# Optimization experiments

Hardware: AMD Instinct MI355X
Metric: run time of the kernel (lower is better)

Reference implementation:

```python
import jax, jax.numpy as jnp
import numpy as np

N_EMBED = 384
NUM_HEADS = 6
HEAD_SIZE = N_EMBED // NUM_HEADS  # 64
B, T = 8, 2048


def setup_inputs() -> dict:
    key = jax.random.key(0)
    ks = jax.random.split(key, 8)
    s = 1.0 / np.sqrt(N_EMBED)
    query = jax.random.normal(ks[0], (B, T, N_EMBED), dtype=jnp.float32)
    key_t = jax.random.normal(ks[1], (B, T, N_EMBED), dtype=jnp.float32)
    value = jax.random.normal(ks[2], (B, T, N_EMBED), dtype=jnp.float32)
    # causal-style mask, broadcastable over (B, H)
    mask = jnp.tril(jnp.ones((T, T), dtype=jnp.int32))[None, None]
    Wk = jax.random.normal(ks[3], (N_EMBED, N_EMBED), dtype=jnp.float32) * s
    Wq = jax.random.normal(ks[4], (N_EMBED, N_EMBED), dtype=jnp.float32) * s
    Wv = jax.random.normal(ks[5], (N_EMBED, N_EMBED), dtype=jnp.float32) * s
    Wproj = jax.random.normal(ks[6], (N_EMBED, N_EMBED), dtype=jnp.float32) * s
    bproj = jnp.zeros((N_EMBED,), dtype=jnp.float32)
    return {"query": query, "key": key_t, "value": value, "mask": mask,
            "Wk": Wk, "Wq": Wq, "Wv": Wv, "Wproj": Wproj, "bproj": bproj}


def _split_heads(x):
    b, t, c = x.shape
    return x.reshape(b, t, NUM_HEADS, c // NUM_HEADS).transpose(0, 2, 1, 3)  # [B,H,T,D]


def reference(query, key, value, mask, Wk, Wq, Wv, Wproj, bproj):
    b, t, c = query.shape
    # NOTE: source swaps names: k = key_proj(query), q = query_proj(key)
    k = _split_heads(query @ Wk.T)
    q = _split_heads(key @ Wq.T)
    v = _split_heads(value @ Wv.T)
    # scale by full C (not head_size), as in the source
    wei = jnp.einsum("bhqd,bhkd->bhqk", q, k) * (c ** -0.5)
    # masked_fill with 0 BEFORE softmax (faithful to source)
    wei = jnp.where(mask == 0, jnp.float32(0.0), wei)
    wei = jax.nn.softmax(wei, axis=-1)
    out = jnp.einsum("bhqk,bhkd->bhqd", wei, v)
    out = out.transpose(0, 2, 1, 3).reshape(b, t, c)
    out = out @ Wproj.T + bproj  # dropout is identity at inference
    return out
```

## Files before the change

### kernel.cpp

```cpp
#include <hip/hip_runtime.h>
#include <hip/hip_bf16.h>
#include <type_traits>


#define TT 2048
#define CC 384
#define HH 6
#define DD 64
#define SCALE2 0.07362223f

#if __has_builtin(__builtin_amdgcn_exp2f)
#define EXP2(x) __builtin_amdgcn_exp2f(x)
#else
#define EXP2(x) exp2f(x)
#endif

typedef __bf16 bf16x8 __attribute__((ext_vector_type(8)));
typedef __bf16 bf16x4 __attribute__((ext_vector_type(4)));
typedef float f32x4 __attribute__((ext_vector_type(4)));

__device__ __forceinline__ int swz(int row, int byteInRow) {
    return row * 128 + (byteInRow ^ ((row & 7) << 4));
}

__global__ __launch_bounds__(256) void qkv_proj_kernel(
    const float* __restrict__ query, const float* __restrict__ key,
    const float* __restrict__ value, const float* __restrict__ Wk,
    const float* __restrict__ Wq, const float* __restrict__ Wv,
    __bf16* __restrict__ Kb, __bf16* __restrict__ Qb, __bf16* __restrict__ VTb)
{
    __shared__ __align__(16) char smem[49152];

    const int tid = threadIdx.x;
    const int wid = tid >> 6, lane = tid & 63;
    const int lrow = lane & 15, g = lane >> 4;
    const int pid = blockIdx.z;
    const int m0 = blockIdx.x * 128, n0 = blockIdx.y * 64;
    const float* X = (pid == 0) ? query : ((pid == 1) ? key : value);
    const float* W = (pid == 0) ? Wk : ((pid == 1) ? Wq : Wv);

    const int xrow = tid >> 4, xcol = (tid & 15) * 4;
    const float* xp = X + (size_t)(m0 + xrow) * CC + xcol;
    const float* wp = W + (size_t)(n0 + (tid >> 4)) * CC + xcol;

    f32x4 xr[8], wr[4];

    f32x4 acc[2][4];
#pragma unroll
    for (int i = 0; i < 2; ++i)
#pragma unroll
        for (int j = 0; j < 4; ++j) acc[i][j] = (f32x4){0.f, 0.f, 0.f, 0.f};

#pragma unroll
    for (int i = 0; i < 8; ++i) xr[i] = *(const f32x4*)(xp + (size_t)i * 16 * CC);
#pragma unroll
    for (int i = 0; i < 4; ++i) wr[i] = *(const f32x4*)(wp + (size_t)i * 16 * CC);
    {
        char* Xd = smem;
        char* Wd = smem + 32768;
#pragma unroll
        for (int i = 0; i < 8; ++i) {
            bf16x4 hh;
            hh[0] = (__bf16)xr[i][0]; hh[1] = (__bf16)xr[i][1];
            hh[2] = (__bf16)xr[i][2]; hh[3] = (__bf16)xr[i][3];
            *(bf16x4*)(Xd + swz(xrow + i * 16, xcol * 2)) = hh;
        }
#pragma unroll
        for (int i = 0; i < 4; ++i) {
            bf16x4 hh;
            hh[0] = (__bf16)wr[i][0]; hh[1] = (__bf16)wr[i][1];
            hh[2] = (__bf16)wr[i][2]; hh[3] = (__bf16)wr[i][3];
            *(bf16x4*)(Wd + swz((tid >> 4) + i * 16, xcol * 2)) = hh;
        }
    }
    __syncthreads();

    int cur = 0;
    for (int kk = 0; kk < 6; ++kk) {
        if (kk < 5) {
            const int k0 = (kk + 1) * 64;
#pragma unroll
            for (int i = 0; i < 8; ++i) xr[i] = *(const f32x4*)(xp + (size_t)i * 16 * CC + k0);
#pragma unroll
            for (int i = 0; i < 4; ++i) wr[i] = *(const f32x4*)(wp + (size_t)i * 16 * CC + k0);
        }
        const char* Xs = smem + cur * 16384;
        const char* Ws = smem + 32768 + cur * 8192;

        __builtin_amdgcn_s_setprio(1);
        if (pid < 2) {
#pragma unroll
            for (int kc = 0; kc < 2; ++kc) {
                int kb = kc * 64 + g * 16;
                bf16x8 a0 = *(bf16x8*)(Xs + swz(wid * 32 + lrow, kb));
                bf16x8 a1 = *(bf16x8*)(Xs + swz(wid * 32 + 16 + lrow, kb));
#pragma unroll
                for (int nf = 0; nf < 4; ++nf) {
                    bf16x8 b = *(bf16x8*)(Ws + swz(nf * 16 + lrow, kb));
                    acc[0][nf] = __builtin_amdgcn_mfma_f32_16x16x32_bf16(a0, b, acc[0][nf], 0, 0, 0);
                    acc[1][nf] = __builtin_amdgcn_mfma_f32_16x16x32_bf16(a1, b, acc[1][nf], 0, 0, 0);
                }
            }
        } else {
#pragma unroll
            for (int kc = 0; kc < 2; ++kc) {
                int kb = kc * 64 + g * 16;
                bf16x8 b0 = *(bf16x8*)(Xs + swz(wid * 32 + lrow, kb));
                bf16x8 b1 = *(bf16x8*)(Xs + swz(wid * 32 + 16 + lrow, kb));
#pragma unroll
                for (int nf = 0; nf < 4; ++nf) {
                    bf16x8 a = *(bf16x8*)(Ws + swz(nf * 16 + lrow, kb));
                    acc[0][nf] = __builtin_amdgcn_mfma_f32_16x16x32_bf16(a, b0, acc[0][nf], 0, 0, 0);
                    acc[1][nf] = __builtin_amdgcn_mfma_f32_16x16x32_bf16(a, b1, acc[1][nf], 0, 0, 0);
                }
            }
        }
        __builtin_amdgcn_s_setprio(0);

        if (kk < 5) {
            char* Xd = smem + (cur ^ 1) * 16384;
            char* Wd = smem + 32768 + (cur ^ 1) * 8192;
#pragma unroll
            for (int i = 0; i < 8; ++i) {
                bf16x4 hh;
                hh[0] = (__bf16)xr[i][0]; hh[1] = (__bf16)xr[i][1];
                hh[2] = (__bf16)xr[i][2]; hh[3] = (__bf16)xr[i][3];
                *(bf16x4*)(Xd + swz(xrow + i * 16, xcol * 2)) = hh;
            }
#pragma unroll
            for (int i = 0; i < 4; ++i) {
                bf16x4 hh;
                hh[0] = (__bf16)wr[i][0]; hh[1] = (__bf16)wr[i][1];
                hh[2] = (__bf16)wr[i][2]; hh[3] = (__bf16)wr[i][3];
                *(bf16x4*)(Wd + swz((tid >> 4) + i * 16, xcol * 2)) = hh;
            }
        }
        __syncthreads();
        cur ^= 1;
    }

    if (pid < 2) {
        __bf16* out = (pid == 0) ? Kb : Qb;
        const float sc = (pid == 1) ? SCALE2 : 1.0f;
#pragma unroll
        for (int mf = 0; mf < 2; ++mf)
#pragma unroll
            for (int nf = 0; nf < 4; ++nf)
#pragma unroll
                for (int r = 0; r < 4; ++r) {
                    int m = m0 + wid * 32 + mf * 16 + g * 4 + r;
                    int n = n0 + nf * 16 + lrow;
                    int b = m >> 11, t = m & 2047, h = n >> 6, d = n & 63;
                    out[((size_t)(b * HH + h) * TT + t) * DD + d] = (__bf16)(acc[mf][nf][r] * sc);
                }
    } else {
#pragma unroll
        for (int mf = 0; mf < 2; ++mf)
#pragma unroll
            for (int nf = 0; nf < 4; ++nf)
#pragma unroll
                for (int r = 0; r < 4; ++r) {
                    int n = n0 + nf * 16 + g * 4 + r;
                    int m = m0 + wid * 32 + mf * 16 + lrow;
                    int b = m >> 11, t = m & 2047, h = n >> 6, d = n & 63;
                    VTb[((size_t)(b * HH + h) * DD + d) * TT + t] = (__bf16)acc[mf][nf][r];
                }
    }
}

__global__ __launch_bounds__(256) void suffix_kernel(
    const __bf16* __restrict__ VTb, float* __restrict__ Ssuf)
{
    __shared__ float tsum[4][32];
    const int bh = blockIdx.x;
    const int tid = threadIdx.x, wid = tid >> 6, lane = tid & 63;

#pragma unroll
    for (int it = 0; it < 4; ++it) {
        const int dr = blockIdx.y * 16 + wid * 4 + it;
        const __bf16* src = VTb + (size_t)(bh * DD + dr) * TT;
#pragma unroll
        for (int step = 0; step < 4; ++step) {
            bf16x8 v = *(const bf16x8*)(src + step * 512 + lane * 8);
            float sacc = 0.f;
#pragma unroll
            for (int i = 0; i < 8; ++i) sacc += (float)v[i];
            sacc += __shfl_xor(sacc, 1);
            sacc += __shfl_xor(sacc, 2);
            sacc += __shfl_xor(sacc, 4);
            if ((lane & 7) == 0) tsum[wid][step * 8 + (lane >> 3)] = sacc;
        }
        float s2 = 0.f;
        for (int j = 0; j < 32; ++j) {
            float tv = tsum[wid][j];
            if (j >= lane) s2 += tv;
        }
        if (lane <= 32) Ssuf[(size_t)(bh * 33 + lane) * 64 + dr] = s2;
    }
}

__global__ __launch_bounds__(256, 3) void attn_kernel(
    const __bf16* __restrict__ Qb, const __bf16* __restrict__ Kb,
    const __bf16* __restrict__ VTb, const float* __restrict__ Ssuf,
    __bf16* __restrict__ attn)
{
    __shared__ __align__(16) char smem[32768];
    const int tid = threadIdx.x;
    const int wid = tid >> 6, lane = tid & 63;
    const int lrow = lane & 15, g = lane >> 4;

    const int i = blockIdx.x;
    const int xcd = i & 7;
    const int j = i >> 3;
    const int rank = j / 6;
    const int bh = xcd * 6 + (j % 6);
    const int Qt = 15 - rank;
    const int q0 = Qt * 128;
    const int nkt = 2 * Qt + 2;

    const int qloc = wid * 32 + lrow;
    const __bf16* qp = Qb + ((size_t)bh * TT + q0 + qloc) * DD + g * 8;
    bf16x8 qb[2][2];
    qb[0][0] = *(const bf16x8*)(qp);
    qb[0][1] = *(const bf16x8*)(qp + 32);
    qb[1][0] = *(const bf16x8*)(qp + 16 * DD);
    qb[1][1] = *(const bf16x8*)(qp + 16 * DD + 32);

    bf16x8 onesf;
#pragma unroll
    for (int ii = 0; ii < 8; ++ii) onesf[ii] = (__bf16)1.0f;

    const int r0 = tid >> 3;
    const int c8 = (tid & 7) * 8;
    const __bf16* kbase = Kb + (size_t)bh * TT * DD;
    const __bf16* vbase = VTb + (size_t)bh * DD * TT;

    bf16x8 kr0, kr1, vr0, vr1;

    f32x4 o[2][4];
#pragma unroll
    for (int mf = 0; mf < 2; ++mf)
#pragma unroll
        for (int ds = 0; ds < 4; ++ds) o[mf][ds] = (f32x4){0.f, 0.f, 0.f, 0.f};
    f32x4 zacc[2];
    zacc[0] = (f32x4){0.f, 0.f, 0.f, 0.f};
    zacc[1] = (f32x4){0.f, 0.f, 0.f, 0.f};

    kr0 = *(const bf16x8*)(kbase + (size_t)r0 * DD + c8);
    kr1 = *(const bf16x8*)(kbase + (size_t)(r0 + 32) * DD + c8);
    vr0 = *(const bf16x8*)(vbase + (size_t)r0 * TT + c8);
    vr1 = *(const bf16x8*)(vbase + (size_t)(r0 + 32) * TT + c8);
    {
        char* Kd = smem;
        char* Vd = smem + 16384;
        *(bf16x8*)(Kd + swz(r0, c8 * 2)) = kr0;
        *(bf16x8*)(Kd + swz(r0 + 32, c8 * 2)) = kr1;
        *(bf16x8*)(Vd + swz(r0, c8 * 2)) = vr0;
        *(bf16x8*)(Vd + swz(r0 + 32, c8 * 2)) = vr1;
    }
    __syncthreads();

    int cur = 0;
    auto body = [&](int kt, auto dmc) {
        constexpr bool DM = decltype(dmc)::value;
        if (kt + 1 < nkt) {
            const int n0 = (kt + 1) * 64;
            kr0 = *(const bf16x8*)(kbase + (size_t)(n0 + r0) * DD + c8);
            kr1 = *(const bf16x8*)(kbase + (size_t)(n0 + r0 + 32) * DD + c8);
            vr0 = *(const bf16x8*)(vbase + (size_t)r0 * TT + n0 + c8);
            vr1 = *(const bf16x8*)(vbase + (size_t)(r0 + 32) * TT + n0 + c8);
        }
        const char* Kc = smem + cur * 8192;
        const char* Vc = smem + 16384 + cur * 8192;

        bf16x8 kfr[2][4];
#pragma unroll
        for (int kc = 0; kc < 2; ++kc)
#pragma unroll
            for (int j16 = 0; j16 < 4; ++j16)
                kfr[kc][j16] = *(const bf16x8*)(Kc + swz(j16 * 16 + lrow, kc * 64 + g * 16));

        f32x4 st[2][4];
#pragma unroll
        for (int mf = 0; mf < 2; ++mf)
#pragma unroll
            for (int j16 = 0; j16 < 4; ++j16) st[mf][j16] = (f32x4){0.f, 0.f, 0.f, 0.f};
        __builtin_amdgcn_s_setprio(1);
#pragma unroll
        for (int kc = 0; kc < 2; ++kc)
#pragma unroll
            for (int mf = 0; mf < 2; ++mf)
#pragma unroll
                for (int j16 = 0; j16 < 4; ++j16)
                    st[mf][j16] = __builtin_amdgcn_mfma_f32_16x16x32_bf16(
                        kfr[kc][j16], qb[mf][kc], st[mf][j16], 0, 0, 0);
        __builtin_amdgcn_s_setprio(0);

        bf16x8 vfr[2][4];
#pragma unroll
        for (int kc = 0; kc < 2; ++kc)
#pragma unroll
            for (int ds = 0; ds < 4; ++ds) {
                union { bf16x8 v8; bf16x4 h[2]; } u;
                u.h[0] = *(const bf16x4*)(Vc + swz(ds * 16 + lrow, kc * 64 + 8 * g));
                u.h[1] = *(const bf16x4*)(Vc + swz(ds * 16 + lrow, kc * 64 + 8 * g + 32));
                vfr[kc][ds] = u.v8;
            }

#pragma unroll
        for (int mf = 0; mf < 2; ++mf) {
            const int qg = q0 + qloc + mf * 16;
            bf16x8 pb0, pb1;
#pragma unroll
            for (int j16 = 0; j16 < 4; ++j16) {
#pragma unroll
                for (int r = 0; r < 4; ++r) {
                    float p;
                    if (DM && (kt * 64 + j16 * 16 + g * 4 + r > qg)) p = 1.0f;
                    else p = EXP2(st[mf][j16][r]);
                    if (j16 < 2) pb0[(j16 & 1) * 4 + r] = (__bf16)p;
                    else         pb1[(j16 & 1) * 4 + r] = (__bf16)p;
                }
            }

            __builtin_amdgcn_s_setprio(1);
#pragma unroll
            for (int kc = 0; kc < 2; ++kc) {
                bf16x8 pf = kc ? pb1 : pb0;
#pragma unroll
                for (int ds = 0; ds < 4; ++ds)
                    o[mf][ds] = __builtin_amdgcn_mfma_f32_16x16x32_bf16(
                        vfr[kc][ds], pf, o[mf][ds], 0, 0, 0);
                zacc[mf] = __builtin_amdgcn_mfma_f32_16x16x32_bf16(
                    onesf, pf, zacc[mf], 0, 0, 0);
            }
            __builtin_amdgcn_s_setprio(0);
        }

        if (kt + 1 < nkt) {
            char* Kd = smem + (cur ^ 1) * 8192;
            char* Vd = smem + 16384 + (cur ^ 1) * 8192;
            *(bf16x8*)(Kd + swz(r0, c8 * 2)) = kr0;
            *(bf16x8*)(Kd + swz(r0 + 32, c8 * 2)) = kr1;
            *(bf16x8*)(Vd + swz(r0, c8 * 2)) = vr0;
            *(bf16x8*)(Vd + swz(r0 + 32, c8 * 2)) = vr1;
        }
        __syncthreads();
        cur ^= 1;
    };

    int kt = 0;
    for (; kt < nkt - 2; ++kt) body(kt, std::false_type{});
    for (; kt < nkt; ++kt) body(kt, std::true_type{});

    const float fut = (float)(TT - nkt * 64);
    const float inv0 = 1.0f / (zacc[0][0] + fut);
    const float inv1 = 1.0f / (zacc[1][0] + fut);

    const float* suf = Ssuf + ((size_t)bh * 33 + nkt) * 64;
    const int b = bh / HH, h = bh % HH;
#pragma unroll
    for (int mf = 0; mf < 2; ++mf) {
        const int t = q0 + qloc + mf * 16;
        const float inv = mf ? inv1 : inv0;
        __bf16* orow = attn + ((size_t)(b * TT + t)) * CC + h * DD;
#pragma unroll
        for (int ds = 0; ds < 4; ++ds) {
            f32x4 sv = *(const f32x4*)(suf + ds * 16 + g * 4);
            bf16x4 w;
#pragma unroll
            for (int r = 0; r < 4; ++r) w[r] = (__bf16)((o[mf][ds][r] + sv[r]) * inv);
            *(bf16x4*)(orow + ds * 16 + g * 4) = w;
        }
    }
}

__global__ __launch_bounds__(256) void out_proj_kernel(
    const __bf16* __restrict__ A, const float* __restrict__ W,
    const float* __restrict__ bias, float* __restrict__ out)
{
    __shared__ __align__(16) char smem[49152];
    const int tid = threadIdx.x;
    const int wid = tid >> 6, lane = tid & 63;
    const int lrow = lane & 15, g = lane >> 4;
    const int m0 = blockIdx.x * 128, n0 = blockIdx.y * 64;

    const int arow = tid >> 3, ac8 = (tid & 7) * 8;
    const __bf16* ap = A + (size_t)(m0 + arow) * CC + ac8;
    const int wrow = tid >> 4, wcol = (tid & 15) * 4;
    const float* wp = W + (size_t)(n0 + wrow) * CC + wcol;

    bf16x8 ar[4];
    f32x4 wr[4];

    f32x4 acc[2][4];
#pragma unroll
    for (int i = 0; i < 2; ++i)
#pragma unroll
        for (int j = 0; j < 4; ++j) acc[i][j] = (f32x4){0.f, 0.f, 0.f, 0.f};

#pragma unroll
    for (int i = 0; i < 4; ++i) ar[i] = *(const bf16x8*)(ap + (size_t)i * 32 * CC);
#pragma unroll
    for (int i = 0; i < 4; ++i) wr[i] = *(const f32x4*)(wp + (size_t)i * 16 * CC);
    {
        char* Ad = smem;
        char* Wd = smem + 32768;
#pragma unroll
        for (int i = 0; i < 4; ++i)
            *(bf16x8*)(Ad + swz(arow + i * 32, ac8 * 2)) = ar[i];
#pragma unroll
        for (int i = 0; i < 4; ++i) {
            bf16x4 hh;
            hh[0] = (__bf16)wr[i][0]; hh[1] = (__bf16)wr[i][1];
            hh[2] = (__bf16)wr[i][2]; hh[3] = (__bf16)wr[i][3];
            *(bf16x4*)(Wd + swz(wrow + i * 16, wcol * 2)) = hh;
        }
    }
    __syncthreads();

    int cur = 0;
    for (int kk = 0; kk < 6; ++kk) {
        if (kk < 5) {
            const int k0 = (kk + 1) * 64;
#pragma unroll
            for (int i = 0; i < 4; ++i) ar[i] = *(const bf16x8*)(ap + (size_t)i * 32 * CC + k0);
#pragma unroll
            for (int i = 0; i < 4; ++i) wr[i] = *(const f32x4*)(wp + (size_t)i * 16 * CC + k0);
        }
        const char* Xs = smem + cur * 16384;
        const char* Ws = smem + 32768 + cur * 8192;

        __builtin_amdgcn_s_setprio(1);
#pragma unroll
        for (int kc = 0; kc < 2; ++kc) {
            int kb = kc * 64 + g * 16;
            bf16x8 a0 = *(bf16x8*)(Xs + swz(wid * 32 + lrow, kb));
            bf16x8 a1 = *(bf16x8*)(Xs + swz(wid * 32 + 16 + lrow, kb));
#pragma unroll
            for (int nf = 0; nf < 4; ++nf) {
                bf16x8 b = *(bf16x8*)(Ws + swz(nf * 16 + lrow, kb));
                acc[0][nf] = __builtin_amdgcn_mfma_f32_16x16x32_bf16(a0, b, acc[0][nf], 0, 0, 0);
                acc[1][nf] = __builtin_amdgcn_mfma_f32_16x16x32_bf16(a1, b, acc[1][nf], 0, 0, 0);
            }
        }
        __builtin_amdgcn_s_setprio(0);

        if (kk < 5) {
            char* Ad = smem + (cur ^ 1) * 16384;
            char* Wd = smem + 32768 + (cur ^ 1) * 8192;
#pragma unroll
            for (int i = 0; i < 4; ++i)
                *(bf16x8*)(Ad + swz(arow + i * 32, ac8 * 2)) = ar[i];
#pragma unroll
            for (int i = 0; i < 4; ++i) {
                bf16x4 hh;
                hh[0] = (__bf16)wr[i][0]; hh[1] = (__bf16)wr[i][1];
                hh[2] = (__bf16)wr[i][2]; hh[3] = (__bf16)wr[i][3];
                *(bf16x4*)(Wd + swz(wrow + i * 16, wcol * 2)) = hh;
            }
        }
        __syncthreads();
        cur ^= 1;
    }

#pragma unroll
    for (int nf = 0; nf < 4; ++nf) {
        float bv = bias[n0 + nf * 16 + lrow];
#pragma unroll
        for (int mf = 0; mf < 2; ++mf)
#pragma unroll
            for (int r = 0; r < 4; ++r) {
                int m = m0 + wid * 32 + mf * 16 + g * 4 + r;
                out[(size_t)m * CC + n0 + nf * 16 + lrow] = acc[mf][nf][r] + bv;
            }
    }
}

extern "C" void kernel_launch(void* const* d_in, const int* in_sizes, int n_in,
                              void* d_out, int out_size, void* d_ws, size_t ws_size,
                              hipStream_t stream)
{
    (void)in_sizes; (void)n_in; (void)out_size; (void)ws_size;
    const float* query = (const float*)d_in[0];
    const float* key   = (const float*)d_in[1];
    const float* value = (const float*)d_in[2];
    const float* Wk    = (const float*)d_in[4];
    const float* Wq    = (const float*)d_in[5];
    const float* Wv    = (const float*)d_in[6];
    const float* Wproj = (const float*)d_in[7];
    const float* bproj = (const float*)d_in[8];
    float* out = (float*)d_out;

    char* ws = (char*)d_ws;
    const size_t SZ = 12582912;
    __bf16* Qb   = (__bf16*)(ws);
    __bf16* Kb   = (__bf16*)(ws + SZ);
    __bf16* VTb  = (__bf16*)(ws + 2 * SZ);
    __bf16* Ab   = (__bf16*)(ws + 3 * SZ);
    float*  Ssuf = (float*)(ws + 4 * SZ);

    qkv_proj_kernel<<<dim3(128, 6, 3), 256, 0, stream>>>(query, key, value,
                                                         Wk, Wq, Wv, Kb, Qb, VTb);
    suffix_kernel<<<dim3(48, 4), 256, 0, stream>>>(VTb, Ssuf);
    attn_kernel<<<dim3(768), 256, 0, stream>>>(Qb, Kb, VTb, Ssuf, Ab);
    out_proj_kernel<<<dim3(128, 6), 256, 0, stream>>>(Ab, Wproj, bproj, out);
}
```

Before: 232.7 us.

## Enlarge projection GEMM tiles to 128x128 with 2x2 warp layout

```diff
diff --git a/kernel.cpp b/kernel.cpp
--- a/kernel.cpp
+++ b/kernel.cpp
@@ -29,32 +29,33 @@
     const float* __restrict__ Wq, const float* __restrict__ Wv,
     __bf16* __restrict__ Kb, __bf16* __restrict__ Qb, __bf16* __restrict__ VTb)
 {
-    __shared__ __align__(16) char smem[49152];
+    __shared__ __align__(16) char smem[65536];
 
     const int tid = threadIdx.x;
     const int wid = tid >> 6, lane = tid & 63;
     const int lrow = lane & 15, g = lane >> 4;
+    const int wrv = wid >> 1, wcv = wid & 1;
     const int pid = blockIdx.z;
-    const int m0 = blockIdx.x * 128, n0 = blockIdx.y * 64;
+    const int m0 = blockIdx.x * 128, n0 = blockIdx.y * 128;
     const float* X = (pid == 0) ? query : ((pid == 1) ? key : value);
     const float* W = (pid == 0) ? Wk : ((pid == 1) ? Wq : Wv);
 
-    const int xrow = tid >> 4, xcol = (tid & 15) * 4;
-    const float* xp = X + (size_t)(m0 + xrow) * CC + xcol;
-    const float* wp = W + (size_t)(n0 + (tid >> 4)) * CC + xcol;
-
-    f32x4 xr[8], wr[4];
-
-    f32x4 acc[2][4];
-#pragma unroll
-    for (int i = 0; i < 2; ++i)
-#pragma unroll
-        for (int j = 0; j < 4; ++j) acc[i][j] = (f32x4){0.f, 0.f, 0.f, 0.f};
+    const int srow = tid >> 4, scol = (tid & 15) * 4;
+    const float* xp = X + (size_t)(m0 + srow) * CC + scol;
+    const float* wp = W + (size_t)(n0 + srow) * CC + scol;
+
+    f32x4 xr[8], wv[8];
+
+    f32x4 acc[4][4];
+#pragma unroll
+    for (int a = 0; a < 4; ++a)
+#pragma unroll
+        for (int bq = 0; bq < 4; ++bq) acc[a][bq] = (f32x4){0.f, 0.f, 0.f, 0.f};
 
 #pragma unroll
     for (int i = 0; i < 8; ++i) xr[i] = *(const f32x4*)(xp + (size_t)i * 16 * CC);
 #pragma unroll
-    for (int i = 0; i < 4; ++i) wr[i] = *(const f32x4*)(wp + (size_t)i * 16 * CC);
+    for (int i = 0; i < 8; ++i) wv[i] = *(const f32x4*)(wp + (size_t)i * 16 * CC);
     {
         char* Xd = smem;
         char* Wd = smem + 32768;
@@ -63,14 +64,14 @@
             bf16x4 hh;
             hh[0] = (__bf16)xr[i][0]; hh[1] = (__bf16)xr[i][1];
             hh[2] = (__bf16)xr[i][2]; hh[3] = (__bf16)xr[i][3];
-            *(bf16x4*)(Xd + swz(xrow + i * 16, xcol * 2)) = hh;
-        }
-#pragma unroll
-        for (int i = 0; i < 4; ++i) {
+            *(bf16x4*)(Xd + swz(srow + i * 16, scol * 2)) = hh;
+        }
+#pragma unroll
+        for (int i = 0; i < 8; ++i) {
             bf16x4 hh;
-            hh[0] = (__bf16)wr[i][0]; hh[1] = (__bf16)wr[i][1];
-            hh[2] = (__bf16)wr[i][2]; hh[3] = (__bf16)wr[i][3];
-            *(bf16x4*)(Wd + swz((tid >> 4) + i * 16, xcol * 2)) = hh;
+            hh[0] = (__bf16)wv[i][0]; hh[1] = (__bf16)wv[i][1];
+            hh[2] = (__bf16)wv[i][2]; hh[3] = (__bf16)wv[i][3];
+            *(bf16x4*)(Wd + swz(srow + i * 16, scol * 2)) = hh;
         }
     }
     __syncthreads();
@@ -82,57 +83,55 @@
 #pragma unroll
             for (int i = 0; i < 8; ++i) xr[i] = *(const f32x4*)(xp + (size_t)i * 16 * CC + k0);
 #pragma unroll
-            for (int i = 0; i < 4; ++i) wr[i] = *(const f32x4*)(wp + (size_t)i * 16 * CC + k0);
+            for (int i = 0; i < 8; ++i) wv[i] = *(const f32x4*)(wp + (size_t)i * 16 * CC + k0);
         }
         const char* Xs = smem + cur * 16384;
-        const char* Ws = smem + 32768 + cur * 8192;
+        const char* Ws = smem + 32768 + cur * 16384;
 
         __builtin_amdgcn_s_setprio(1);
-        if (pid < 2) {
-#pragma unroll
-            for (int kc = 0; kc < 2; ++kc) {
-                int kb = kc * 64 + g * 16;
-                bf16x8 a0 = *(bf16x8*)(Xs + swz(wid * 32 + lrow, kb));
-                bf16x8 a1 = *(bf16x8*)(Xs + swz(wid * 32 + 16 + lrow, kb));
-#pragma unroll
-                for (int nf = 0; nf < 4; ++nf) {
-                    bf16x8 b = *(bf16x8*)(Ws + swz(nf * 16 + lrow, kb));
-                    acc[0][nf] = __builtin_amdgcn_mfma_f32_16x16x32_bf16(a0, b, acc[0][nf], 0, 0, 0);
-                    acc[1][nf] = __builtin_amdgcn_mfma_f32_16x16x32_bf16(a1, b, acc[1][nf], 0, 0, 0);
-                }
-            }
-        } else {
-#pragma unroll
-            for (int kc = 0; kc < 2; ++kc) {
-                int kb = kc * 64 + g * 16;
-                bf16x8 b0 = *(bf16x8*)(Xs + swz(wid * 32 + lrow, kb));
-                bf16x8 b1 = *(bf16x8*)(Xs + swz(wid * 32 + 16 + lrow, kb));
-#pragma unroll
-                for (int nf = 0; nf < 4; ++nf) {
-                    bf16x8 a = *(bf16x8*)(Ws + swz(nf * 16 + lrow, kb));
-                    acc[0][nf] = __builtin_amdgcn_mfma_f32_16x16x32_bf16(a, b0, acc[0][nf], 0, 0, 0);
-                    acc[1][nf] = __builtin_amdgcn_mfma_f32_16x16x32_bf16(a, b1, acc[1][nf], 0, 0, 0);
-                }
+#pragma unroll
+        for (int kc = 0; kc < 2; ++kc) {
+            const int kb = kc * 64 + g * 16;
+            bf16x8 xf[4], wf[4];
+#pragma unroll
+            for (int t4 = 0; t4 < 4; ++t4) {
+                xf[t4] = *(const bf16x8*)(Xs + swz(wrv * 64 + t4 * 16 + lrow, kb));
+                wf[t4] = *(const bf16x8*)(Ws + swz(wcv * 64 + t4 * 16 + lrow, kb));
+            }
+            if (pid < 2) {
+#pragma unroll
+                for (int mf = 0; mf < 4; ++mf)
+#pragma unroll
+                    for (int nf = 0; nf < 4; ++nf)
+                        acc[mf][nf] = __builtin_amdgcn_mfma_f32_16x16x32_bf16(
+                            xf[mf], wf[nf], acc[mf][nf], 0, 0, 0);
+            } else {
+#pragma unroll
+                for (int nf = 0; nf < 4; ++nf)
+#pragma unroll
+                    for (int mf = 0; mf < 4; ++mf)
+                        acc[nf][mf] = __builtin_amdgcn_mfma_f32_16x16x32_bf16(
+                            wf[nf], xf[mf], acc[nf][mf], 0, 0, 0);
             }
         }
         __builtin_amdgcn_s_setprio(0);
 
         if (kk < 5) {
             char* Xd = smem + (cur ^ 1) * 16384;
-            char* Wd = smem + 32768 + (cur ^ 1) * 8192;
+            char* Wd = smem + 32768 + (cur ^ 1) * 16384;
 #pragma unroll
             for (int i = 0; i < 8; ++i) {
                 bf16x4 hh;
                 hh[0] = (__bf16)xr[i][0]; hh[1] = (__bf16)xr[i][1];
                 hh[2] = (__bf16)xr[i][2]; hh[3] = (__bf16)xr[i][3];
-                *(bf16x4*)(Xd + swz(xrow + i * 16, xcol * 2)) = hh;
-            }
-#pragma unroll
-            for (int i = 0; i < 4; ++i) {
+                *(bf16x4*)(Xd + swz(srow + i * 16, scol * 2)) = hh;
+            }
+#pragma unroll
+            for (int i = 0; i < 8; ++i) {
                 bf16x4 hh;
-                hh[0] = (__bf16)wr[i][0]; hh[1] = (__bf16)wr[i][1];
-                hh[2] = (__bf16)wr[i][2]; hh[3] = (__bf16)wr[i][3];
-                *(bf16x4*)(Wd + swz((tid >> 4) + i * 16, xcol * 2)) = hh;
+                hh[0] = (__bf16)wv[i][0]; hh[1] = (__bf16)wv[i][1];
+                hh[2] = (__bf16)wv[i][2]; hh[3] = (__bf16)wv[i][3];
+                *(bf16x4*)(Wd + swz(srow + i * 16, scol * 2)) = hh;
             }
         }
         __syncthreads();
@@ -143,27 +142,27 @@
         __bf16* out = (pid == 0) ? Kb : Qb;
         const float sc = (pid == 1) ? SCALE2 : 1.0f;
 #pragma unroll
-        for (int mf = 0; mf < 2; ++mf)
+        for (int mf = 0; mf < 4; ++mf)
 #pragma unroll
             for (int nf = 0; nf < 4; ++nf)
 #pragma unroll
                 for (int r = 0; r < 4; ++r) {
-                    int m = m0 + wid * 32 + mf * 16 + g * 4 + r;
-                    int n = n0 + nf * 16 + lrow;
+                    int m = m0 + wrv * 64 + mf * 16 + g * 4 + r;
+                    int n = n0 + wcv * 64 + nf * 16 + lrow;
                     int b = m >> 11, t = m & 2047, h = n >> 6, d = n & 63;
                     out[((size_t)(b * HH + h) * TT + t) * DD + d] = (__bf16)(acc[mf][nf][r] * sc);
                 }
     } else {
 #pragma unroll
-        for (int mf = 0; mf < 2; ++mf)
-#pragma unroll
-            for (int nf = 0; nf < 4; ++nf)
+        for (int nf = 0; nf < 4; ++nf)
+#pragma unroll
+            for (int mf = 0; mf < 4; ++mf)
 #pragma unroll
                 for (int r = 0; r < 4; ++r) {
-                    int n = n0 + nf * 16 + g * 4 + r;
-                    int m = m0 + wid * 32 + mf * 16 + lrow;
+                    int n = n0 + wcv * 64 + nf * 16 + g * 4 + r;
+                    int m = m0 + wrv * 64 + mf * 16 + lrow;
                     int b = m >> 11, t = m & 2047, h = n >> 6, d = n & 63;
-                    VTb[((size_t)(b * HH + h) * DD + d) * TT + t] = (__bf16)acc[mf][nf][r];
+                    VTb[((size_t)(b * HH + h) * DD + d) * TT + t] = (__bf16)acc[nf][mf][r];
                 }
     }
 }
@@ -379,30 +378,31 @@
     const __bf16* __restrict__ A, const float* __restrict__ W,
     const float* __restrict__ bias, float* __restrict__ out)
 {
-    __shared__ __align__(16) char smem[49152];
+    __shared__ __align__(16) char smem[65536];
     const int tid = threadIdx.x;
     const int wid = tid >> 6, lane = tid & 63;
     const int lrow = lane & 15, g = lane >> 4;
-    const int m0 = blockIdx.x * 128, n0 = blockIdx.y * 64;
+    const int wrv = wid >> 1, wcv = wid & 1;
+    const int m0 = blockIdx.x * 128, n0 = blockIdx.y * 128;
 
     const int arow = tid >> 3, ac8 = (tid & 7) * 8;
     const __bf16* ap = A + (size_t)(m0 + arow) * CC + ac8;
-    const int wrow = tid >> 4, wcol = (tid & 15) * 4;
-    const float* wp = W + (size_t)(n0 + wrow) * CC + wcol;
+    const int wsr = tid >> 4, wscol = (tid & 15) * 4;
+    const float* wp = W + (size_t)(n0 + wsr) * CC + wscol;
 
     bf16x8 ar[4];
-    f32x4 wr[4];
-
-    f32x4 acc[2][4];
-#pragma unroll
-    for (int i = 0; i < 2; ++i)
-#pragma unroll
-        for (int j = 0; j < 4; ++j) acc[i][j] = (f32x4){0.f, 0.f, 0.f, 0.f};
+    f32x4 wv[8];
+
+    f32x4 acc[4][4];
+#pragma unroll
+    for (int a = 0; a < 4; ++a)
+#pragma unroll
+        for (int bq = 0; bq < 4; ++bq) acc[a][bq] = (f32x4){0.f, 0.f, 0.f, 0.f};
 
 #pragma unroll
     for (int i = 0; i < 4; ++i) ar[i] = *(const bf16x8*)(ap + (size_t)i * 32 * CC);
 #pragma unroll
-    for (int i = 0; i < 4; ++i) wr[i] = *(const f32x4*)(wp + (size_t)i * 16 * CC);
+    for (int i = 0; i < 8; ++i) wv[i] = *(const f32x4*)(wp + (size_t)i * 16 * CC);
     {
         char* Ad = smem;
         char* Wd = smem + 32768;
@@ -410,11 +410,11 @@
         for (int i = 0; i < 4; ++i)
             *(bf16x8*)(Ad + swz(arow + i * 32, ac8 * 2)) = ar[i];
 #pragma unroll
-        for (int i = 0; i < 4; ++i) {
+        for (int i = 0; i < 8; ++i) {
             bf16x4 hh;
-            hh[0] = (__bf16)wr[i][0]; hh[1] = (__bf16)wr[i][1];
-            hh[2] = (__bf16)wr[i][2]; hh[3] = (__bf16)wr[i][3];
-            *(bf16x4*)(Wd + swz(wrow + i * 16, wcol * 2)) = hh;
+            hh[0] = (__bf16)wv[i][0]; hh[1] = (__bf16)wv[i][1];
+            hh[2] = (__bf16)wv[i][2]; hh[3] = (__bf16)wv[i][3];
+            *(bf16x4*)(Wd + swz(wsr + i * 16, wscol * 2)) = hh;
         }
     }
     __syncthreads();
@@ -426,38 +426,42 @@
 #pragma unroll
             for (int i = 0; i < 4; ++i) ar[i] = *(const bf16x8*)(ap + (size_t)i * 32 * CC + k0);
 #pragma unroll
-            for (int i = 0; i < 4; ++i) wr[i] = *(const f32x4*)(wp + (size_t)i * 16 * CC + k0);
+            for (int i = 0; i < 8; ++i) wv[i] = *(const f32x4*)(wp + (size_t)i * 16 * CC + k0);
         }
         const char* Xs = smem + cur * 16384;
-        const char* Ws = smem + 32768 + cur * 8192;
+        const char* Ws = smem + 32768 + cur * 16384;
 
         __builtin_amdgcn_s_setprio(1);
 #pragma unroll
         for (int kc = 0; kc < 2; ++kc) {
-            int kb = kc * 64 + g * 16;
-            bf16x8 a0 = *(bf16x8*)(Xs + swz(wid * 32 + lrow, kb));
-            bf16x8 a1 = *(bf16x8*)(Xs + swz(wid * 32 + 16 + lrow, kb));
-#pragma unroll
-            for (int nf = 0; nf < 4; ++nf) {
-                bf16x8 b = *(bf16x8*)(Ws + swz(nf * 16 + lrow, kb));
-                acc[0][nf] = __builtin_amdgcn_mfma_f32_16x16x32_bf16(a0, b, acc[0][nf], 0, 0, 0);
-                acc[1][nf] = __builtin_amdgcn_mfma_f32_16x16x32_bf16(a1, b, acc[1][nf], 0, 0, 0);
-            }
+            const int kb = kc * 64 + g * 16;
+            bf16x8 af[4], bf[4];
+#pragma unroll
+            for (int t4 = 0; t4 < 4; ++t4) {
+                af[t4] = *(const bf16x8*)(Xs + swz(wrv * 64 + t4 * 16 + lrow, kb));
+                bf[t4] = *(const bf16x8*)(Ws + swz(wcv * 64 + t4 * 16 + lrow, kb));
+            }
+#pragma unroll
+            for (int mf = 0; mf < 4; ++mf)
+#pragma unroll
+                for (int nf = 0; nf < 4; ++nf)
+                    acc[mf][nf] = __builtin_amdgcn_mfma_f32_16x16x32_bf16(
+                        af[mf], bf[nf], acc[mf][nf], 0, 0, 0);
         }
         __builtin_amdgcn_s_setprio(0);
 
         if (kk < 5) {
             char* Ad = smem + (cur ^ 1) * 16384;
-            char* Wd = smem + 32768 + (cur ^ 1) * 8192;
+            char* Wd = smem + 32768 + (cur ^ 1) * 16384;
 #pragma unroll
             for (int i = 0; i < 4; ++i)
                 *(bf16x8*)(Ad + swz(arow + i * 32, ac8 * 2)) = ar[i];
 #pragma unroll
-            for (int i = 0; i < 4; ++i) {
+            for (int i = 0; i < 8; ++i) {
                 bf16x4 hh;
-                hh[0] = (__bf16)wr[i][0]; hh[1] = (__bf16)wr[i][1];
-                hh[2] = (__bf16)wr[i][2]; hh[3] = (__bf16)wr[i][3];
-                *(bf16x4*)(Wd + swz(wrow + i * 16, wcol * 2)) = hh;
+                hh[0] = (__bf16)wv[i][0]; hh[1] = (__bf16)wv[i][1];
+                hh[2] = (__bf16)wv[i][2]; hh[3] = (__bf16)wv[i][3];
+                *(bf16x4*)(Wd + swz(wsr + i * 16, wscol * 2)) = hh;
             }
         }
         __syncthreads();
@@ -466,13 +470,13 @@
 
 #pragma unroll
     for (int nf = 0; nf < 4; ++nf) {
-        float bv = bias[n0 + nf * 16 + lrow];
-#pragma unroll
-        for (int mf = 0; mf < 2; ++mf)
+        float bv = bias[n0 + wcv * 64 + nf * 16 + lrow];
+#pragma unroll
+        for (int mf = 0; mf < 4; ++mf)
 #pragma unroll
             for (int r = 0; r < 4; ++r) {
-                int m = m0 + wid * 32 + mf * 16 + g * 4 + r;
-                out[(size_t)m * CC + n0 + nf * 16 + lrow] = acc[mf][nf][r] + bv;
+                int m = m0 + wrv * 64 + mf * 16 + g * 4 + r;
+                out[(size_t)m * CC + n0 + wcv * 64 + nf * 16 + lrow] = acc[mf][nf][r] + bv;
             }
     }
 }
@@ -500,9 +504,9 @@
     __bf16* Ab   = (__bf16*)(ws + 3 * SZ);
     float*  Ssuf = (float*)(ws + 4 * SZ);
 
-    qkv_proj_kernel<<<dim3(128, 6, 3), 256, 0, stream>>>(query, key, value,
+    qkv_proj_kernel<<<dim3(128, 3, 3), 256, 0, stream>>>(query, key, value,
                                                          Wk, Wq, Wv, Kb, Qb, VTb);
     suffix_kernel<<<dim3(48, 4), 256, 0, stream>>>(VTb, Ssuf);
     attn_kernel<<<dim3(768), 256, 0, stream>>>(Qb, Kb, VTb, Ssuf, Ab);
-    out_proj_kernel<<<dim3(128, 6), 256, 0, stream>>>(Ab, Wproj, bproj, out);
+    out_proj_kernel<<<dim3(128, 3), 256, 0, stream>>>(Ab, Wproj, bproj, out);
 }
```

Result: faster. 224.4 us (-3.5%).
